# Performance work log

Measured on AMD Instinct MI355X. Metric: run time of the kernel, lower is better.

Reference implementation:

```python
import jax, jax.numpy as jnp
import numpy as np

B, S, DM, H, HD = 2, 4096, 768, 12, 64   # longformer-base-4096
W = 256    # one-sided attention window (attention_window=512)
NB = S // W
G = 16     # number of leading global-attention tokens ([CLS]+query)
OUT = 512  # hidden_dim of final fc


def setup_inputs() -> dict:
    key = jax.random.key(0)
    ks = jax.random.split(key, 11)
    def w(k, shape):
        return jax.random.normal(k, shape, jnp.float32) * 0.02
    z = lambda n: jnp.zeros((n,), jnp.float32)
    return {
        "x": jax.random.normal(ks[0], (B, S, DM), jnp.float32),
        "wq": w(ks[1], (DM, DM)), "bq": z(DM),
        "wk": w(ks[2], (DM, DM)), "bk": z(DM),
        "wv": w(ks[3], (DM, DM)), "bv": z(DM),
        "wqg": w(ks[4], (DM, DM)), "bqg": z(DM),
        "wkg": w(ks[5], (DM, DM)), "bkg": z(DM),
        "wvg": w(ks[6], (DM, DM)), "bvg": z(DM),
        "wo": w(ks[7], (DM, DM)), "bo": z(DM),
        "wp": w(ks[8], (DM, DM)), "bp": z(DM),
        "wfc": w(ks[9], (DM, OUT)), "bfc": z(OUT),
    }


def _longformer_forward(x, wq, bq, wk, bk, wv, bv, wqg, bqg, wkg, bkg,
                        wvg, bvg, wo, bo, wp, bp, wfc, bfc):
    scale = jnp.float32(1.0 / np.sqrt(HD))
    q = ((x @ wq + bq) * scale).reshape(B, S, H, HD)
    k = (x @ wk + bk).reshape(B, S, H, HD)
    v = (x @ wv + bv).reshape(B, S, H, HD)

    # --- sliding-window (banded) attention via overlapping key/value blocks ---
    kp = jnp.pad(k, ((0, 0), (W, W), (0, 0), (0, 0)))  # [B, S+2W, H, HD]
    vp = jnp.pad(v, ((0, 0), (W, W), (0, 0), (0, 0)))
    blk = jnp.arange(NB)[:, None] * W + jnp.arange(3 * W)[None, :]  # [NB,3W]
    kb = kp[:, blk]  # [B, NB, 3W, H, HD]
    vb = vp[:, blk]
    qb = q.reshape(B, NB, W, H, HD)
    sc_loc = jnp.einsum('bnqhd,bnkhd->bhnqk', qb, kb)  # [B,H,NB,W,3W]

    i = jnp.arange(W)[:, None]
    j = jnp.arange(3 * W)[None, :]
    band = (j >= i) & (j <= i + 2 * W)                       # |rel| <= W
    abs_k = (jnp.arange(NB)[:, None, None] - 1) * W + j[None]  # [NB,W,3W]
    # mask padding, out-of-band, and global keys (handled separately per HF)
    valid = band[None] & (abs_k >= 0) & (abs_k < S) & (abs_k >= G)
    sc_loc = jnp.where(valid[None, None], sc_loc, jnp.float32(-1e9))

    # every query also attends to the G global keys (regular k/v per HF)
    sc_glb = jnp.einsum('bqhd,bghd->bhqg', q, k[:, :G])  # [B,H,S,G]

    sc = jnp.concatenate([sc_glb, sc_loc.reshape(B, H, S, 3 * W)], axis=-1)
    p = jax.nn.softmax(sc, axis=-1)
    p_g, p_l = p[..., :G], p[..., G:]
    out = jnp.einsum('bhqg,bghd->bqhd', p_g, v[:, :G])
    out = out + jnp.einsum('bhnqk,bnkhd->bnqhd',
                           p_l.reshape(B, H, NB, W, 3 * W), vb).reshape(B, S, H, HD)

    # --- global queries: full attention with the dedicated global projections ---
    qg = ((x[:, :G] @ wqg + bqg) * scale).reshape(B, G, H, HD)
    kg = (x @ wkg + bkg).reshape(B, S, H, HD)
    vg = (x @ wvg + bvg).reshape(B, S, H, HD)
    pg = jax.nn.softmax(jnp.einsum('bghd,bshd->bhgs', qg, kg), axis=-1)
    out_g = jnp.einsum('bhgs,bshd->bghd', pg, vg)
    out = jnp.concatenate([out_g, out[:, G:]], axis=1)

    attn = out.reshape(B, S, DM) @ wo + bo
    pooled = jnp.tanh(attn[:, 0] @ wp + bp)  # HF pooler on [CLS]
    return pooled @ wfc + bfc                # final nn.Linear -> [B, OUT]


def reference(x, wq, bq, wk, bk, wv, bv, wqg, bqg, wkg, bkg, wvg, bvg,
              wo, bo, wp, bp, wfc, bfc):
    return _longformer_forward(x, wq, bq, wk, bk, wv, bv, wqg, bqg, wkg,
                               bkg, wvg, bvg, wo, bo, wp, bp, wfc, bfc)
```

## Files before the change

### kernel.cpp

```cpp
#include <hip/hip_runtime.h>
#include <hip/hip_bf16.h>

#define BB 2
#define SS 4096
#define DM 768
#define NH 12
#define OUTC 512
#define QSCALE 0.125f
#define NCHUNK 128
#define CS 32
#define HPB 3
#define HG  (NH/HPB)
#define JSA 4
#define JWA (DM/JSA)
#define JT 64
#define JR (DM/JT)

__device__ __forceinline__ float wave_sum64(float v) {
#pragma unroll
  for (int o = 32; o > 0; o >>= 1) v += __shfl_xor(v, o, 64);
  return v;
}

__global__ __launch_bounds__(256) void kA(const float* __restrict__ x,
    const float* __restrict__ wqg, const float* __restrict__ bqg,
    const float* __restrict__ wkg, const float* __restrict__ bkg,
    float* __restrict__ qw_ws, float* __restrict__ qb_ws,
    float* __restrict__ l_ws, float* __restrict__ xw_ws) {
  int h = blockIdx.x, b = blockIdx.y, js = blockIdx.z, t = threadIdx.x;
  __shared__ float x0[DM];
  __shared__ float4 red4[16][16];
  __shared__ float qg0[64];
  for (int i = t; i < DM; i += 256) x0[i] = x[(size_t)b*SS*DM + i];
  for (int i = t; i < JWA; i += 256)
    xw_ws[((size_t)b*NH + h)*DM + js*JWA + i] = 0.f;
  if (js == 0 && t == 0) l_ws[b*NH + h] = 0.f;
  __syncthreads();
  {
    int cq = t & 15, jg = t >> 4;
    const float4* wq4 = (const float4*)wqg;
    float4 a = {0.f, 0.f, 0.f, 0.f};
#pragma unroll 8
    for (int jo = 0; jo < 48; ++jo) {
      int j = jg*48 + jo;
      float xv = x0[j];
      float4 wv = wq4[(size_t)j*(DM/4) + h*16 + cq];
      a.x += xv*wv.x; a.y += xv*wv.y; a.z += xv*wv.z; a.w += xv*wv.w;
    }
    red4[jg][cq] = a;
  }
  __syncthreads();
  if (t < 16) {
    float4 a = {0.f, 0.f, 0.f, 0.f};
#pragma unroll
    for (int jg = 0; jg < 16; ++jg) {
      float4 r = red4[jg][t];
      a.x += r.x; a.y += r.y; a.z += r.z; a.w += r.w;
    }
    float4 bq = ((const float4*)(bqg + h*64))[t];
    a.x = (a.x + bq.x)*QSCALE; a.y = (a.y + bq.y)*QSCALE;
    a.z = (a.z + bq.z)*QSCALE; a.w = (a.w + bq.w)*QSCALE;
    ((float4*)qg0)[t] = a;
  }
  __syncthreads();
  if (js == 0 && t < 64) {
    float v = wave_sum64(qg0[t] * bkg[h*64 + t]);
    if (t == 0) qb_ws[b*NH + h] = v;
  }
  const float4* qg4 = (const float4*)qg0;
  for (int jj = t; jj < JWA; jj += 256) {
    int j = js*JWA + jj;
    const float4* wr = (const float4*)(wkg + (size_t)j*DM + h*64);
    float acc = 0.f;
#pragma unroll
    for (int q = 0; q < 16; ++q) {
      float4 wv = wr[q], qv = qg4[q];
      acc += wv.x*qv.x + wv.y*qv.y + wv.z*qv.z + wv.w*qv.w;
    }
    qw_ws[((size_t)b*NH + h)*DM + j] = acc;
  }
}

__global__ __launch_bounds__(256) void kB(const float* __restrict__ x,
    const float* __restrict__ qw_ws, const float* __restrict__ qb_ws,
    float* __restrict__ l_ws, float* __restrict__ xw_ws) {
  int chunk = blockIdx.x, b = blockIdx.y, h0 = blockIdx.z * HPB;
  int t = threadIdx.x, lane = t & 63, w = t >> 6;
  __shared__ alignas(16) float qw[HPB*DM];
  __shared__ float qb[HPB];
  __shared__ alignas(16) float pl[CS*HPB];
  for (int i = t; i < HPB*DM; i += 256) qw[i] = qw_ws[((size_t)b*NH + h0)*DM + i];
  if (t < HPB) qb[t] = qb_ws[b*NH + h0 + t];
  __syncthreads();
  const size_t xbase = ((size_t)b*SS + chunk*CS) * DM;
  const float4* x4 = (const float4*)(x + xbase);
  const float4* qw4 = (const float4*)qw;
  float lacc = 0.f;

  for (int batch = 0; batch < 2; ++batch) {
    int sl = w*8 + batch*4;
    float acc[4][HPB];
#pragma unroll
    for (int si = 0; si < 4; ++si)
#pragma unroll
      for (int hh = 0; hh < HPB; ++hh) acc[si][hh] = 0.f;
#pragma unroll
    for (int k = 0; k < 3; ++k) {
      int jq = k*64 + lane;
      float4 xf[4];
#pragma unroll
      for (int si = 0; si < 4; ++si)
        xf[si] = x4[(size_t)(sl + si)*192 + jq];
#pragma unroll
      for (int hh = 0; hh < HPB; ++hh) {
        float4 qv = qw4[hh*192 + jq];
#pragma unroll
        for (int si = 0; si < 4; ++si)
          acc[si][hh] += xf[si].x*qv.x + xf[si].y*qv.y + xf[si].z*qv.z + xf[si].w*qv.w;
      }
    }
    float preg = 0.f;
#pragma unroll
    for (int si = 0; si < 4; ++si)
#pragma unroll
      for (int hh = 0; hh < HPB; ++hh) {
        float r = wave_sum64(acc[si][hh]);
        float pp = __expf(r + qb[hh]);
        if (lane == hh) lacc += pp;
        if (lane == si*HPB + hh) preg = pp;
      }
    if (lane < 4*HPB) pl[(sl + lane/HPB)*HPB + (lane % HPB)] = preg;
  }
  if (lane < HPB) atomicAdd(&l_ws[b*NH + h0 + lane], lacc);
  __syncthreads();

  float a2[HPB][3];
#pragma unroll
  for (int hh = 0; hh < HPB; ++hh)
#pragma unroll
    for (int i = 0; i < 3; ++i) a2[hh][i] = 0.f;
  for (int s = 0; s < CS; ++s) {
    float pv[HPB];
#pragma unroll
    for (int hh = 0; hh < HPB; ++hh) pv[hh] = pl[s*HPB + hh];
    float xv[3];
#pragma unroll
    for (int i = 0; i < 3; ++i)
      xv[i] = x[xbase + (size_t)s*DM + t + 256*i];
#pragma unroll
    for (int hh = 0; hh < HPB; ++hh)
#pragma unroll
      for (int i = 0; i < 3; ++i) a2[hh][i] += pv[hh]*xv[i];
  }
#pragma unroll
  for (int hh = 0; hh < HPB; ++hh)
#pragma unroll
    for (int i = 0; i < 3; ++i)
      atomicAdd(&xw_ws[((size_t)b*NH + h0 + hh)*DM + t + 256*i], a2[hh][i]);
}

__global__ __launch_bounds__(256) void kE1(const float* __restrict__ xw_ws,
    const float* __restrict__ l_ws, const float* __restrict__ wvg,
    const float* __restrict__ bvg, float* __restrict__ out0_ws,
    float* __restrict__ zbuf) {
  int h = blockIdx.x, b = blockIdx.y, t = threadIdx.x;
  __shared__ float xws[DM];
  __shared__ float4 red4[16][16];
  int bid = b*NH + h;
  if (t < 128) zbuf[bid*128 + t] = 0.f;
  float inv = 1.f / l_ws[bid];
#pragma unroll
  for (int i = 0; i < 3; ++i) {
    int j = t + 256*i;
    xws[j] = xw_ws[((size_t)b*NH + h)*DM + j] * inv;
  }
  __syncthreads();
  {
    int cq = t & 15, jg = t >> 4;
    const float4* wv4 = (const float4*)wvg;
    float4 a = {0.f, 0.f, 0.f, 0.f};
#pragma unroll 8
    for (int jo = 0; jo < 48; ++jo) {
      int j = jg*48 + jo;
      float xv = xws[j];
      float4 wv = wv4[(size_t)j*(DM/4) + h*16 + cq];
      a.x += xv*wv.x; a.y += xv*wv.y; a.z += xv*wv.z; a.w += xv*wv.w;
    }
    red4[jg][cq] = a;
  }
  __syncthreads();
  if (t < 16) {
    float4 a = {0.f, 0.f, 0.f, 0.f};
#pragma unroll
    for (int jg = 0; jg < 16; ++jg) {
      float4 r = red4[jg][t];
      a.x += r.x; a.y += r.y; a.z += r.z; a.w += r.w;
    }
    float4 bv = ((const float4*)(bvg + h*64))[t];
    a.x += bv.x; a.y += bv.y; a.z += bv.z; a.w += bv.w;
    ((float4*)(out0_ws + (size_t)b*DM + h*64))[t] = a;
  }
}

__global__ __launch_bounds__(192) void kT(const float* __restrict__ inraw,
    const float* __restrict__ bias, const float* __restrict__ W,
    float* __restrict__ outacc) {
  int jb = blockIdx.x, t = threadIdx.x;
  __shared__ float xs[2][JR];
  int j0 = jb*JR;
  if (t < 2*JR) {
    int bb = t / JR, jj = t % JR;
    float v = inraw[bb*DM + j0 + jj];
    if (bias) v += bias[j0 + jj];
    xs[bb][jj] = v;
  }
  __syncthreads();
  float4 a0 = {0,0,0,0}, a1 = {0,0,0,0};
  const float4* W4 = (const float4*)W;
#pragma unroll
  for (int jj = 0; jj < JR; ++jj) {
    float4 wv = W4[(size_t)(j0 + jj)*192 + t];
    float s0 = xs[0][jj], s1 = xs[1][jj];
    a0.x += s0*wv.x; a0.y += s0*wv.y; a0.z += s0*wv.z; a0.w += s0*wv.w;
    a1.x += s1*wv.x; a1.y += s1*wv.y; a1.z += s1*wv.z; a1.w += s1*wv.w;
  }
  int c = t*4;
  atomicAdd(&outacc[c+0], a0.x); atomicAdd(&outacc[c+1], a0.y);
  atomicAdd(&outacc[c+2], a0.z); atomicAdd(&outacc[c+3], a0.w);
  atomicAdd(&outacc[DM+c+0], a1.x); atomicAdd(&outacc[DM+c+1], a1.y);
  atomicAdd(&outacc[DM+c+2], a1.z); atomicAdd(&outacc[DM+c+3], a1.w);
}

__global__ __launch_bounds__(256) void kT3(const float* __restrict__ pooledraw,
    const float* __restrict__ bp, const float* __restrict__ wfc,
    const float* __restrict__ bfc, float* __restrict__ out) {
  int tile = blockIdx.x, b = blockIdx.y, t = threadIdx.x;
  __shared__ float pls[DM];
  __shared__ float4 red4[16][16];
  for (int i = t; i < DM; i += 256) pls[i] = tanhf(pooledraw[b*DM + i] + bp[i]);
  __syncthreads();
  {
    int cq = t & 15, jg = t >> 4;
    const float4* w4 = (const float4*)wfc;
    float4 a = {0.f, 0.f, 0.f, 0.f};
#pragma unroll 8
    for (int jo = 0; jo < 48; ++jo) {
      int j = jg*48 + jo;
      float pv = pls[j];
      float4 wv = w4[(size_t)j*(OUTC/4) + tile*16 + cq];
      a.x += pv*wv.x; a.y += pv*wv.y; a.z += pv*wv.z; a.w += pv*wv.w;
    }
    red4[jg][cq] = a;
  }
  __syncthreads();
  if (t < 16) {
    float4 a = {0.f, 0.f, 0.f, 0.f};
#pragma unroll
    for (int jg = 0; jg < 16; ++jg) {
      float4 r = red4[jg][t];
      a.x += r.x; a.y += r.y; a.z += r.z; a.w += r.w;
    }
    float4 bf = ((const float4*)(bfc + tile*64))[t];
    a.x += bf.x; a.y += bf.y; a.z += bf.z; a.w += bf.w;
    ((float4*)(out + (size_t)b*OUTC + tile*64))[t] = a;
  }
}

extern "C" void kernel_launch(void* const* d_in, const int* in_sizes, int n_in,
                              void* d_out, int out_size, void* d_ws, size_t ws_size,
                              hipStream_t stream) {
  const float* x   = (const float*)d_in[0];
  const float* wqg = (const float*)d_in[7];
  const float* bqg = (const float*)d_in[8];
  const float* wkg = (const float*)d_in[9];
  const float* bkg = (const float*)d_in[10];
  const float* wvg = (const float*)d_in[11];
  const float* bvg = (const float*)d_in[12];
  const float* wo  = (const float*)d_in[13];
  const float* bo  = (const float*)d_in[14];
  const float* wp  = (const float*)d_in[15];
  const float* bp  = (const float*)d_in[16];
  const float* wfc = (const float*)d_in[17];
  const float* bfc = (const float*)d_in[18];

  float* ws        = (float*)d_ws;
  float* qw        = ws;
  float* qb        = ws + 18432;
  float* l         = ws + 18456;
  float* xw        = ws + 18480;
  float* out0      = ws + 36912;
  float* attnraw   = ws + 38448;
  float* pooledraw = ws + 39984;

  kA <<<dim3(NH, BB, JSA), 256, 0, stream>>>(x, wqg, bqg, wkg, bkg, qw, qb, l, xw);
  kB <<<dim3(NCHUNK, BB, HG), 256, 0, stream>>>(x, qw, qb, l, xw);
  kE1<<<dim3(NH, BB),     256, 0, stream>>>(xw, l, wvg, bvg, out0, attnraw);
  kT <<<dim3(JT),         192, 0, stream>>>(out0, nullptr, wo, attnraw);
  kT <<<dim3(JT),         192, 0, stream>>>(attnraw, bo, wp, pooledraw);
  kT3<<<dim3(8, BB),      256, 0, stream>>>(pooledraw, bp, wfc, bfc, (float*)d_out);
}
```

Before: 192.1 us.

## Process all heads per chunk and replace atomic accumulation with partial buffers

Adds a new global-attention pass in which each block handles all 12 heads for a 16-row chunk of x. Each slice of x is then read once instead of once per head group. The block writes per-chunk weighted-x partials to a large workspace instead of issuing many global atomicAdds into xw. A split-K version of the value-projection kernel reduces those partials and combines results with a small number of atomics into out0, which kA now zeroes. The cost is an extra ~19MB write and read of the partial buffer and more LDS and register use per block. The old path is kept as a fallback for when the workspace is too small.

New measurement: 173.1 us. -9.9%, faster.

```diff
diff --git a/kernel.cpp b/kernel.cpp
--- a/kernel.cpp
+++ b/kernel.cpp
@@ -1,5 +1,4 @@
 #include <hip/hip_runtime.h>
-#include <hip/hip_bf16.h>
 
 #define BB 2
 #define SS 4096
@@ -7,14 +6,17 @@
 #define NH 12
 #define OUTC 512
 #define QSCALE 0.125f
-#define NCHUNK 128
-#define CS 32
-#define HPB 3
-#define HG  (NH/HPB)
+
+#define MCHUNK 256
+#define MCS 16
 #define JSA 4
 #define JWA (DM/JSA)
 #define JT 64
 #define JR (DM/JT)
+#define NCHUNK 128
+#define CS 32
+#define HPB 3
+#define HG (NH/HPB)
 
 __device__ __forceinline__ float wave_sum64(float v) {
 #pragma unroll
@@ -26,7 +28,8 @@
     const float* __restrict__ wqg, const float* __restrict__ bqg,
     const float* __restrict__ wkg, const float* __restrict__ bkg,
     float* __restrict__ qw_ws, float* __restrict__ qb_ws,
-    float* __restrict__ l_ws, float* __restrict__ xw_ws) {
+    float* __restrict__ l_ws, float* __restrict__ xw_ws,
+    float* __restrict__ zb ) {
   int h = blockIdx.x, b = blockIdx.y, js = blockIdx.z, t = threadIdx.x;
   __shared__ float x0[DM];
   __shared__ float4 red4[16][16];
@@ -34,12 +37,13 @@
   for (int i = t; i < DM; i += 256) x0[i] = x[(size_t)b*SS*DM + i];
   for (int i = t; i < JWA; i += 256)
     xw_ws[((size_t)b*NH + h)*DM + js*JWA + i] = 0.f;
+  if (js == 3 && t < 192) zb[(b*NH + h)*192 + t] = 0.f;
   if (js == 0 && t == 0) l_ws[b*NH + h] = 0.f;
   __syncthreads();
   {
     int cq = t & 15, jg = t >> 4;
     const float4* wq4 = (const float4*)wqg;
-    float4 a = {0.f, 0.f, 0.f, 0.f};
+    float4 a = {0,0,0,0};
 #pragma unroll 8
     for (int jo = 0; jo < 48; ++jo) {
       int j = jg*48 + jo;
@@ -51,7 +55,7 @@
   }
   __syncthreads();
   if (t < 16) {
-    float4 a = {0.f, 0.f, 0.f, 0.f};
+    float4 a = {0,0,0,0};
 #pragma unroll
     for (int jg = 0; jg < 16; ++jg) {
       float4 r = red4[jg][t];
@@ -81,108 +85,107 @@
   }
 }
 
-__global__ __launch_bounds__(256) void kB(const float* __restrict__ x,
+__global__ __launch_bounds__(256) void kBp(const float* __restrict__ x,
     const float* __restrict__ qw_ws, const float* __restrict__ qb_ws,
-    float* __restrict__ l_ws, float* __restrict__ xw_ws) {
-  int chunk = blockIdx.x, b = blockIdx.y, h0 = blockIdx.z * HPB;
-  int t = threadIdx.x, lane = t & 63, w = t >> 6;
-  __shared__ alignas(16) float qw[HPB*DM];
-  __shared__ float qb[HPB];
-  __shared__ alignas(16) float pl[CS*HPB];
-  for (int i = t; i < HPB*DM; i += 256) qw[i] = qw_ws[((size_t)b*NH + h0)*DM + i];
-  if (t < HPB) qb[t] = qb_ws[b*NH + h0 + t];
-  __syncthreads();
-  const size_t xbase = ((size_t)b*SS + chunk*CS) * DM;
+    float* __restrict__ l_ws, float* __restrict__ part) {
+  const int chunk = blockIdx.x, b = blockIdx.y;
+  const int t = threadIdx.x, lane = t & 63, w = t >> 6;
+  __shared__ alignas(16) float qw[NH*DM];
+  __shared__ float qb[NH];
+  __shared__ alignas(16) float pl[MCS*NH];
+  __shared__ float lred[4][NH];
+  const float4* qwsrc = (const float4*)(qw_ws + (size_t)b*NH*DM);
+  float4* qw4s = (float4*)qw;
+#pragma unroll
+  for (int i = 0; i < 9; ++i) qw4s[t + 256*i] = qwsrc[t + 256*i];
+  if (t < NH) qb[t] = qb_ws[b*NH + t];
+  __syncthreads();
+  const size_t xbase = ((size_t)b*SS + (size_t)chunk*MCS) * DM;
   const float4* x4 = (const float4*)(x + xbase);
   const float4* qw4 = (const float4*)qw;
-  float lacc = 0.f;
-
-  for (int batch = 0; batch < 2; ++batch) {
-    int sl = w*8 + batch*4;
-    float acc[4][HPB];
+  const int sl = w*4;
+  float acc[4][NH];
+#pragma unroll
+  for (int si = 0; si < 4; ++si)
+#pragma unroll
+    for (int hh = 0; hh < NH; ++hh) acc[si][hh] = 0.f;
+#pragma unroll
+  for (int k = 0; k < 3; ++k) {
+    int jq = k*64 + lane;
+    float4 xf[4];
 #pragma unroll
     for (int si = 0; si < 4; ++si)
-#pragma unroll
-      for (int hh = 0; hh < HPB; ++hh) acc[si][hh] = 0.f;
-#pragma unroll
-    for (int k = 0; k < 3; ++k) {
-      int jq = k*64 + lane;
-      float4 xf[4];
+      xf[si] = x4[(size_t)(sl + si)*192 + jq];
+#pragma unroll
+    for (int hh = 0; hh < NH; ++hh) {
+      float4 qv = qw4[hh*192 + jq];
 #pragma unroll
       for (int si = 0; si < 4; ++si)
-        xf[si] = x4[(size_t)(sl + si)*192 + jq];
-#pragma unroll
-      for (int hh = 0; hh < HPB; ++hh) {
-        float4 qv = qw4[hh*192 + jq];
-#pragma unroll
-        for (int si = 0; si < 4; ++si)
-          acc[si][hh] += xf[si].x*qv.x + xf[si].y*qv.y + xf[si].z*qv.z + xf[si].w*qv.w;
+        acc[si][hh] += xf[si].x*qv.x + xf[si].y*qv.y + xf[si].z*qv.z + xf[si].w*qv.w;
+    }
+  }
+  float lacc = 0.f, preg = 0.f;
+#pragma unroll
+  for (int si = 0; si < 4; ++si)
+#pragma unroll
+    for (int hh = 0; hh < NH; ++hh) {
+      float r = wave_sum64(acc[si][hh]);
+      float pp = __expf(r + qb[hh]);
+      if (lane == hh) lacc += pp;
+      if (lane == si*NH + hh) preg = pp;
+    }
+  if (lane < 4*NH) pl[sl*NH + lane] = preg;
+  if (lane < NH) lred[w][lane] = lacc;
+  __syncthreads();
+  if (t < NH)
+    atomicAdd(&l_ws[b*NH + t], lred[0][t] + lred[1][t] + lred[2][t] + lred[3][t]);
+  if (t < 192) {
+    float4 a2[NH];
+#pragma unroll
+    for (int hh = 0; hh < NH; ++hh) a2[hh] = make_float4(0.f,0.f,0.f,0.f);
+    for (int s = 0; s < MCS; ++s) {
+      float4 xv = x4[s*192 + t];
+      const float4* p4 = (const float4*)(pl + s*NH);
+      float4 p0 = p4[0], p1 = p4[1], p2 = p4[2];
+      float pv[NH] = {p0.x,p0.y,p0.z,p0.w, p1.x,p1.y,p1.z,p1.w, p2.x,p2.y,p2.z,p2.w};
+#pragma unroll
+      for (int hh = 0; hh < NH; ++hh) {
+        a2[hh].x += pv[hh]*xv.x; a2[hh].y += pv[hh]*xv.y;
+        a2[hh].z += pv[hh]*xv.z; a2[hh].w += pv[hh]*xv.w;
       }
     }
-    float preg = 0.f;
-#pragma unroll
-    for (int si = 0; si < 4; ++si)
-#pragma unroll
-      for (int hh = 0; hh < HPB; ++hh) {
-        float r = wave_sum64(acc[si][hh]);
-        float pp = __expf(r + qb[hh]);
-        if (lane == hh) lacc += pp;
-        if (lane == si*HPB + hh) preg = pp;
-      }
-    if (lane < 4*HPB) pl[(sl + lane/HPB)*HPB + (lane % HPB)] = preg;
-  }
-  if (lane < HPB) atomicAdd(&l_ws[b*NH + h0 + lane], lacc);
-  __syncthreads();
-
-  float a2[HPB][3];
-#pragma unroll
-  for (int hh = 0; hh < HPB; ++hh)
-#pragma unroll
-    for (int i = 0; i < 3; ++i) a2[hh][i] = 0.f;
-  for (int s = 0; s < CS; ++s) {
-    float pv[HPB];
-#pragma unroll
-    for (int hh = 0; hh < HPB; ++hh) pv[hh] = pl[s*HPB + hh];
-    float xv[3];
-#pragma unroll
-    for (int i = 0; i < 3; ++i)
-      xv[i] = x[xbase + (size_t)s*DM + t + 256*i];
-#pragma unroll
-    for (int hh = 0; hh < HPB; ++hh)
-#pragma unroll
-      for (int i = 0; i < 3; ++i) a2[hh][i] += pv[hh]*xv[i];
-  }
-#pragma unroll
-  for (int hh = 0; hh < HPB; ++hh)
-#pragma unroll
-    for (int i = 0; i < 3; ++i)
-      atomicAdd(&xw_ws[((size_t)b*NH + h0 + hh)*DM + t + 256*i], a2[hh][i]);
-}
-
-__global__ __launch_bounds__(256) void kE1(const float* __restrict__ xw_ws,
+    float4* pdst = (float4*)part;
+    const size_t base = (size_t)(b*MCHUNK + chunk)*NH*192;
+#pragma unroll
+    for (int hh = 0; hh < NH; ++hh)
+      pdst[base + (size_t)hh*192 + t] = a2[hh];
+  }
+}
+
+__global__ __launch_bounds__(256) void kE1p(const float* __restrict__ part,
     const float* __restrict__ l_ws, const float* __restrict__ wvg,
-    const float* __restrict__ bvg, float* __restrict__ out0_ws,
-    float* __restrict__ zbuf) {
-  int h = blockIdx.x, b = blockIdx.y, t = threadIdx.x;
-  __shared__ float xws[DM];
+    const float* __restrict__ bvg, float* __restrict__ out0) {
+  int h = blockIdx.x, b = blockIdx.y, js = blockIdx.z, t = threadIdx.x;
+  __shared__ float xws[JWA];
   __shared__ float4 red4[16][16];
-  int bid = b*NH + h;
-  if (t < 128) zbuf[bid*128 + t] = 0.f;
-  float inv = 1.f / l_ws[bid];
-#pragma unroll
-  for (int i = 0; i < 3; ++i) {
-    int j = t + 256*i;
-    xws[j] = xw_ws[((size_t)b*NH + h)*DM + j] * inv;
+  if (t < 192) {
+    float acc = 0.f;
+    const float* src = part + ((size_t)(b*MCHUNK)*NH + h)*DM + (size_t)js*192 + t;
+#pragma unroll 8
+    for (int c = 0; c < MCHUNK; ++c)
+      acc += src[(size_t)c*NH*DM];
+    xws[t] = acc * (1.f / l_ws[b*NH + h]);
   }
   __syncthreads();
   {
     int cq = t & 15, jg = t >> 4;
     const float4* wv4 = (const float4*)wvg;
-    float4 a = {0.f, 0.f, 0.f, 0.f};
-#pragma unroll 8
-    for (int jo = 0; jo < 48; ++jo) {
-      int j = jg*48 + jo;
-      float xv = xws[j];
+    float4 a = {0,0,0,0};
+#pragma unroll
+    for (int jo = 0; jo < 12; ++jo) {
+      int jl = jg*12 + jo;
+      int j = js*192 + jl;
+      float xv = xws[jl];
       float4 wv = wv4[(size_t)j*(DM/4) + h*16 + cq];
       a.x += xv*wv.x; a.y += xv*wv.y; a.z += xv*wv.z; a.w += xv*wv.w;
     }
@@ -190,15 +193,19 @@
   }
   __syncthreads();
   if (t < 16) {
-    float4 a = {0.f, 0.f, 0.f, 0.f};
+    float4 a = {0,0,0,0};
 #pragma unroll
     for (int jg = 0; jg < 16; ++jg) {
       float4 r = red4[jg][t];
       a.x += r.x; a.y += r.y; a.z += r.z; a.w += r.w;
     }
-    float4 bv = ((const float4*)(bvg + h*64))[t];
-    a.x += bv.x; a.y += bv.y; a.z += bv.z; a.w += bv.w;
-    ((float4*)(out0_ws + (size_t)b*DM + h*64))[t] = a;
+    if (js == 0) {
+      float4 bv = ((const float4*)(bvg + h*64))[t];
+      a.x += bv.x; a.y += bv.y; a.z += bv.z; a.w += bv.w;
+    }
+    float* dst = out0 + (size_t)b*DM + h*64 + t*4;
+    atomicAdd(dst+0, a.x); atomicAdd(dst+1, a.y);
+    atomicAdd(dst+2, a.z); atomicAdd(dst+3, a.w);
   }
 }
 
@@ -242,7 +249,7 @@
   {
     int cq = t & 15, jg = t >> 4;
     const float4* w4 = (const float4*)wfc;
-    float4 a = {0.f, 0.f, 0.f, 0.f};
+    float4 a = {0,0,0,0};
 #pragma unroll 8
     for (int jo = 0; jo < 48; ++jo) {
       int j = jg*48 + jo;
@@ -254,7 +261,7 @@
   }
   __syncthreads();
   if (t < 16) {
-    float4 a = {0.f, 0.f, 0.f, 0.f};
+    float4 a = {0,0,0,0};
 #pragma unroll
     for (int jg = 0; jg < 16; ++jg) {
       float4 r = red4[jg][t];
@@ -263,6 +270,126 @@
     float4 bf = ((const float4*)(bfc + tile*64))[t];
     a.x += bf.x; a.y += bf.y; a.z += bf.z; a.w += bf.w;
     ((float4*)(out + (size_t)b*OUTC + tile*64))[t] = a;
+  }
+}
+
+
+__global__ __launch_bounds__(256) void kB(const float* __restrict__ x,
+    const float* __restrict__ qw_ws, const float* __restrict__ qb_ws,
+    float* __restrict__ l_ws, float* __restrict__ xw_ws) {
+  int chunk = blockIdx.x, b = blockIdx.y, h0 = blockIdx.z * HPB;
+  int t = threadIdx.x, lane = t & 63, w = t >> 6;
+  __shared__ alignas(16) float qw[HPB*DM];
+  __shared__ float qb[HPB];
+  __shared__ alignas(16) float pl[CS*HPB];
+  for (int i = t; i < HPB*DM; i += 256) qw[i] = qw_ws[((size_t)b*NH + h0)*DM + i];
+  if (t < HPB) qb[t] = qb_ws[b*NH + h0 + t];
+  __syncthreads();
+  const size_t xbase = ((size_t)b*SS + chunk*CS) * DM;
+  const float4* x4 = (const float4*)(x + xbase);
+  const float4* qw4 = (const float4*)qw;
+  float lacc = 0.f;
+  for (int batch = 0; batch < 2; ++batch) {
+    int sl = w*8 + batch*4;
+    float acc[4][HPB];
+#pragma unroll
+    for (int si = 0; si < 4; ++si)
+#pragma unroll
+      for (int hh = 0; hh < HPB; ++hh) acc[si][hh] = 0.f;
+#pragma unroll
+    for (int k = 0; k < 3; ++k) {
+      int jq = k*64 + lane;
+      float4 xf[4];
+#pragma unroll
+      for (int si = 0; si < 4; ++si)
+        xf[si] = x4[(size_t)(sl + si)*192 + jq];
+#pragma unroll
+      for (int hh = 0; hh < HPB; ++hh) {
+        float4 qv = qw4[hh*192 + jq];
+#pragma unroll
+        for (int si = 0; si < 4; ++si)
+          acc[si][hh] += xf[si].x*qv.x + xf[si].y*qv.y + xf[si].z*qv.z + xf[si].w*qv.w;
+      }
+    }
+    float preg = 0.f;
+#pragma unroll
+    for (int si = 0; si < 4; ++si)
+#pragma unroll
+      for (int hh = 0; hh < HPB; ++hh) {
+        float r = wave_sum64(acc[si][hh]);
+        float pp = __expf(r + qb[hh]);
+        if (lane == hh) lacc += pp;
+        if (lane == si*HPB + hh) preg = pp;
+      }
+    if (lane < 4*HPB) pl[(sl + lane/HPB)*HPB + (lane % HPB)] = preg;
+  }
+  if (lane < HPB) atomicAdd(&l_ws[b*NH + h0 + lane], lacc);
+  __syncthreads();
+  float a2[HPB][3];
+#pragma unroll
+  for (int hh = 0; hh < HPB; ++hh)
+#pragma unroll
+    for (int i = 0; i < 3; ++i) a2[hh][i] = 0.f;
+  for (int s = 0; s < CS; ++s) {
+    float pv[HPB];
+#pragma unroll
+    for (int hh = 0; hh < HPB; ++hh) pv[hh] = pl[s*HPB + hh];
+    float xv[3];
+#pragma unroll
+    for (int i = 0; i < 3; ++i)
+      xv[i] = x[xbase + (size_t)s*DM + t + 256*i];
+#pragma unroll
+    for (int hh = 0; hh < HPB; ++hh)
+#pragma unroll
+      for (int i = 0; i < 3; ++i) a2[hh][i] += pv[hh]*xv[i];
+  }
+#pragma unroll
+  for (int hh = 0; hh < HPB; ++hh)
+#pragma unroll
+    for (int i = 0; i < 3; ++i)
+      atomicAdd(&xw_ws[((size_t)b*NH + h0 + hh)*DM + t + 256*i], a2[hh][i]);
+}
+
+__global__ __launch_bounds__(256) void kE1(const float* __restrict__ xw_ws,
+    const float* __restrict__ l_ws, const float* __restrict__ wvg,
+    const float* __restrict__ bvg, float* __restrict__ out0_ws,
+    float* __restrict__ zbuf) {
+  int h = blockIdx.x, b = blockIdx.y, t = threadIdx.x;
+  __shared__ float xws[DM];
+  __shared__ float4 red4[16][16];
+  int bid = b*NH + h;
+  if (t < 128) zbuf[bid*128 + t] = 0.f;
+  float inv = 1.f / l_ws[bid];
+#pragma unroll
+  for (int i = 0; i < 3; ++i) {
+    int j = t + 256*i;
+    xws[j] = xw_ws[((size_t)b*NH + h)*DM + j] * inv;
+  }
+  __syncthreads();
+  {
+    int cq = t & 15, jg = t >> 4;
+    const float4* wv4 = (const float4*)wvg;
+    float4 a = {0,0,0,0};
+#pragma unroll 8
+    for (int jo = 0; jo < 48; ++jo) {
+      int j = jg*48 + jo;
+      float xv = xws[j];
+      float4 wv = wv4[(size_t)j*(DM/4) + h*16 + cq];
+      a.x += xv*wv.x; a.y += xv*wv.y; a.z += xv*wv.z; a.w += xv*wv.w;
+    }
+    red4[jg][cq] = a;
+  }
+  __syncthreads();
+  if (t < 16) {
+    float4 a = {0,0,0,0};
+#pragma unroll
+    for (int jg = 0; jg < 16; ++jg) {
+      float4 r = red4[jg][t];
+      a.x += r.x; a.y += r.y; a.z += r.z; a.w += r.w;
+    }
+    float4 bv = ((const float4*)(bvg + h*64))[t];
+    a.x += bv.x; a.y += bv.y; a.z += bv.z; a.w += bv.w;
+    ((float4*)(out0_ws + (size_t)b*DM + h*64))[t] = a;
   }
 }
 
@@ -291,11 +418,19 @@
   float* out0      = ws + 36912;
   float* attnraw   = ws + 38448;
   float* pooledraw = ws + 39984;
-
-  kA <<<dim3(NH, BB, JSA), 256, 0, stream>>>(x, wqg, bqg, wkg, bkg, qw, qb, l, xw);
-  kB <<<dim3(NCHUNK, BB, HG), 256, 0, stream>>>(x, qw, qb, l, xw);
-  kE1<<<dim3(NH, BB),     256, 0, stream>>>(xw, l, wvg, bvg, out0, attnraw);
-  kT <<<dim3(JT),         192, 0, stream>>>(out0, nullptr, wo, attnraw);
-  kT <<<dim3(JT),         192, 0, stream>>>(attnraw, bo, wp, pooledraw);
-  kT3<<<dim3(8, BB),      256, 0, stream>>>(pooledraw, bp, wfc, bfc, (float*)d_out);
-}
+  float* part      = ws + 41520;
+
+  const size_t need_bytes = (size_t)(41520 + (size_t)BB*MCHUNK*NH*DM) * sizeof(float);
+
+  kA<<<dim3(NH, BB, JSA), 256, 0, stream>>>(x, wqg, bqg, wkg, bkg, qw, qb, l, xw, out0);
+  if (ws_size >= need_bytes) {
+    kBp <<<dim3(MCHUNK, BB), 256, 0, stream>>>(x, qw, qb, l, part);
+    kE1p<<<dim3(NH, BB, 4),  256, 0, stream>>>(part, l, wvg, bvg, out0);
+  } else {
+    kB  <<<dim3(NCHUNK, BB, HG), 256, 0, stream>>>(x, qw, qb, l, xw);
+    kE1 <<<dim3(NH, BB),         256, 0, stream>>>(xw, l, wvg, bvg, out0, attnraw);
+  }
+  kT <<<dim3(JT),    192, 0, stream>>>(out0, nullptr, wo, attnraw);
+  kT <<<dim3(JT),    192, 0, stream>>>(attnraw, bo, wp, pooledraw);
+  kT3<<<dim3(8, BB), 256, 0, stream>>>(pooledraw, bp, wfc, bfc, (float*)d_out);
+}
```
